# Performance work log

Measured on AMD Instinct MI355X. Metric: run time of the kernel, lower is better.

The kernel has to match this reference:

```python
import jax, jax.numpy as jnp
import numpy as np

N, E, R, D = 100000, 600000, 3, 128  # nodes, edges per relation, relations, hidden


def setup_inputs() -> dict:
    key = jax.random.key(0)
    ks = jax.random.split(key, 12)
    sc = 1.0 / np.sqrt(D)
    return dict(
        x=jax.random.normal(ks[0], (N, D), jnp.float32),
        edge_src=jax.random.randint(ks[1], (R, E), 0, N, jnp.int32),
        edge_dst=jax.random.randint(ks[2], (R, E), 0, N, jnp.int32),
        edge_w=jax.random.uniform(ks[3], (R, E), jnp.float32),
        W=jax.random.normal(ks[4], (R, D, D), jnp.float32) * sc,
        attn_l=jax.random.normal(ks[5], (R, D), jnp.float32) * sc,
        attn_r=jax.random.normal(ks[6], (R, D), jnp.float32) * sc,
        gat_b=jnp.zeros((R, D), jnp.float32),
        bi_w=jax.random.normal(ks[7], (D, D), jnp.float32) * sc,
        bi_b=jnp.zeros((D,), jnp.float32),
        si_w=jax.random.normal(ks[8], (D, D), jnp.float32) * sc,
        si_b=jnp.zeros((D,), jnp.float32),
        res_w=jax.random.normal(ks[9], (), jnp.float32),
        ln_g=jnp.ones((D,), jnp.float32),
        ln_b=jnp.zeros((D,), jnp.float32),
    )


def _leaky(x, slope):
    return jnp.where(x >= 0, x, slope * x)


def _gat(x, W, al, ar, b, src, dst, ew):
    # DGL GATConv, 1 head, edge-weighted: h = xW; e = LReLU(a_l.h_src + a_r.h_dst);
    # alpha = edge_softmax(e per dst) * edge_weight; out[d] = sum alpha * h_src + bias.
    h = x @ W                                   # (N, D)
    el = (h * al).sum(-1)                       # (N,)
    er = (h * ar).sum(-1)                       # (N,)
    e = _leaky(el[src] + er[dst], 0.2)          # (E,)
    m = jax.ops.segment_max(e, dst, num_segments=N)
    a = jnp.exp(e - m[dst])
    s = jax.ops.segment_sum(a, dst, num_segments=N)
    alpha = a / s[dst] * ew                     # (E,)
    out = jax.ops.segment_sum(alpha[:, None] * h[src], dst, num_segments=N)
    return out + b                              # zero-indegree nodes -> bias only


def reference(x, edge_src, edge_dst, edge_w, W, attn_l, attn_r, gat_b,
              bi_w, bi_b, si_w, si_b, res_w, ln_g, ln_b):
    # per-relation intra aggregation, stacked along relation axis: (N, R, D)
    feats = jnp.stack(
        [_gat(x, W[r], attn_l[r], attn_r[r], gat_b[r],
              edge_src[r], edge_dst[r], edge_w[r]) for r in range(R)], axis=1)
    # FM-style bi-interaction over the relation axis
    s = feats.sum(axis=1)                       # (N, D)
    deep_fm = 0.5 * (s ** 2 - (feats ** 2).sum(axis=1))
    nfm = _leaky(deep_fm @ bi_w.T + bi_b, 0.01) + _leaky(s @ si_w.T + si_b, 0.01)
    # gated residual + LayerNorm
    out = nfm + x * jax.nn.sigmoid(res_w)
    mu = out.mean(-1, keepdims=True)
    var = ((out - mu) ** 2).mean(-1, keepdims=True)
    return (out - mu) * jax.lax.rsqrt(var + 1e-5) * ln_g + ln_b
```

## Files before the change

### kernel.cpp

```cpp
#include <hip/hip_runtime.h>

#define DD 128
typedef unsigned int u32;
typedef __attribute__((ext_vector_type(8))) short bf16x8;
typedef __attribute__((ext_vector_type(4))) float f32x4;

__device__ __forceinline__ float lrelu(float v, float s) { return v >= 0.f ? v : s * v; }
__device__ __forceinline__ ushort f2bf(float f) {
  union { float f; u32 u; } v; v.f = f;
  u32 u = v.u;
  return (ushort)((u + 0x7FFFu + ((u >> 16) & 1u)) >> 16);
}
__device__ __forceinline__ float bf2f(ushort s) { return __uint_as_float(((u32)s) << 16); }

union frag_cvt { uint4 u; bf16x8 h; };

__global__ __launch_bounds__(256) void k_prep_w(const float* __restrict__ W,
                                                short* __restrict__ WA)
{
  int t = blockIdx.x * 256 + threadIdx.x;
  int lane = t & 63, ks = (t >> 6) & 3, cf = (t >> 8) & 7, r = t >> 11;
  int c = cf * 16 + (lane & 15);
  int kb = ks * 32 + (lane >> 4) * 8;
  const float* Wr = W + (size_t)r * DD * DD;
  ushort o[8];
#pragma unroll
  for (int j = 0; j < 8; j++) o[j] = f2bf(Wr[(size_t)(kb + j) * DD + c]);
  uint4 st;
  st.x = (u32)o[0] | ((u32)o[1] << 16);
  st.y = (u32)o[2] | ((u32)o[3] << 16);
  st.z = (u32)o[4] | ((u32)o[5] << 16);
  st.w = (u32)o[6] | ((u32)o[7] << 16);
  *(uint4*)(WA + (size_t)t * 8) = st;
}

__global__ __launch_bounds__(256) void k_prep_cw(const float* __restrict__ bw,
                                                 const float* __restrict__ sw,
                                                 short* __restrict__ WB)
{
  int t = blockIdx.x * 256 + threadIdx.x;
  int lane = t & 63, ks = (t >> 6) & 3, cf = (t >> 8) & 7, m = t >> 11;
  const float* src = m ? sw : bw;
  int c = cf * 16 + (lane & 15);
  int k = ks * 32 + (lane >> 4) * 8;
  const float* pr = src + (size_t)c * DD + k;
  uint4 st;
  st.x = (u32)f2bf(pr[0]) | ((u32)f2bf(pr[1]) << 16);
  st.y = (u32)f2bf(pr[2]) | ((u32)f2bf(pr[3]) << 16);
  st.z = (u32)f2bf(pr[4]) | ((u32)f2bf(pr[5]) << 16);
  st.w = (u32)f2bf(pr[6]) | ((u32)f2bf(pr[7]) << 16);
  *(uint4*)(WB + (size_t)t * 8) = st;
}

__global__ void k_prep_av(const float* __restrict__ W, const float* __restrict__ al,
                          const float* __restrict__ ar, float* __restrict__ wl,
                          float* __restrict__ wr)
{
  int t = blockIdx.x * 192 + threadIdx.x;
  if (t >= 384) return;
  int r = t >> 7, k = t & 127;
  const float* Wrow = W + (size_t)r * DD * DD + (size_t)k * DD;
  const float* alr = al + r * DD;
  const float* arr = ar + r * DD;
  float pl = 0.f, pr = 0.f;
  for (int c = 0; c < DD; c++) { float w = Wrow[c]; pl = fmaf(w, alr[c], pl); pr = fmaf(w, arr[c], pr); }
  wl[t] = pl; wr[t] = pr;
}

__global__ __launch_bounds__(256) void k_prep_xrow(
    const float* __restrict__ x, const float* __restrict__ wl, const float* __restrict__ wr,
    u32* __restrict__ xrow, float* __restrict__ el, int2* __restrict__ bex, int N)
{
  const int wid = (int)(((long long)blockIdx.x * 256 + threadIdx.x) >> 6);
  const int lane = threadIdx.x & 63;
  if (wid >= N) return;
  float2 xv = *(const float2*)(x + (size_t)wid * DD + lane * 2);
  xrow[(size_t)wid * 64 + lane] = (u32)f2bf(xv.x) | ((u32)f2bf(xv.y) << 16);
  float d[6];
#pragma unroll
  for (int r = 0; r < 3; r++) {
    float2 wlv = *(const float2*)(wl + r * DD + lane * 2);
    float2 wrv = *(const float2*)(wr + r * DD + lane * 2);
    d[r]     = xv.x * wlv.x + xv.y * wlv.y;
    d[r + 3] = xv.x * wrv.x + xv.y * wrv.y;
  }
#pragma unroll
  for (int o = 32; o; o >>= 1) {
#pragma unroll
    for (int k = 0; k < 6; k++) d[k] += __shfl_xor(d[k], o);
  }
  if (lane == 0) {
#pragma unroll
    for (int r = 0; r < 3; r++) {
      el[(size_t)r * N + wid] = d[r];
      bex[(size_t)r * N + wid].y = __float_as_int(d[r + 3]);
    }
  }
}

__global__ void k_hist3(const int* __restrict__ dst, int* __restrict__ cnt,
                        int* __restrict__ rank, int N, int E) {
  int i = blockIdx.x * 256 + threadIdx.x;
  int r = blockIdx.y;
  if (i < E) {
    size_t ei = (size_t)r * E + i;
    rank[ei] = atomicAdd(cnt + (size_t)r * N + dst[ei], 1);
  }
}

__global__ __launch_bounds__(256) void k_scan_bsum(const int* __restrict__ cnt,
                                                   int* __restrict__ bsum, int M)
{
  __shared__ int red[256];
  const int t = threadIdx.x;
  const int g0 = blockIdx.x * 2048 + t * 8;
  int s = 0;
#pragma unroll
  for (int j = 0; j < 8; j++) { int i = g0 + j; if (i < M) s += cnt[i]; }
  red[t] = s;
  __syncthreads();
  for (int o = 128; o; o >>= 1) {
    if (t < o) red[t] += red[t + o];
    __syncthreads();
  }
  if (t == 0) bsum[blockIdx.x] = red[0];
}

__global__ __launch_bounds__(256) void k_scan_btop(const int* __restrict__ bsum,
                                                   int* __restrict__ bpre, int NB)
{
  __shared__ int sums[256];
  const int t = threadIdx.x;
  int v = (t < NB) ? bsum[t] : 0;
  sums[t] = v;
  __syncthreads();
  for (int o = 1; o < 256; o <<= 1) {
    int u = (t >= o) ? sums[t - o] : 0;
    __syncthreads();
    sums[t] += u;
    __syncthreads();
  }
  if (t < NB) bpre[t] = sums[t] - v;
}

__global__ __launch_bounds__(256) void k_scan_base(const int* __restrict__ cnt,
    const int* __restrict__ bpre, int2* __restrict__ bex, int M)
{
  __shared__ int sums[256];
  const int t = threadIdx.x;
  const int g0 = blockIdx.x * 2048 + t * 8;
  int c[8];
  int ts = 0;
#pragma unroll
  for (int j = 0; j < 8; j++) { int i = g0 + j; c[j] = (i < M) ? cnt[i] : 0; ts += c[j]; }
  sums[t] = ts;
  __syncthreads();
  for (int o = 1; o < 256; o <<= 1) {
    int u = (t >= o) ? sums[t - o] : 0;
    __syncthreads();
    sums[t] += u;
    __syncthreads();
  }
  int run = bpre[blockIdx.x] + sums[t] - ts;
#pragma unroll
  for (int j = 0; j < 8; j++) {
    int i = g0 + j;
    if (i <= M) bex[i].x = run;
    run += c[j];
  }
}

__global__ void k_scatter3(const int* __restrict__ src, const int* __restrict__ dst,
    const float* __restrict__ ew, const float* __restrict__ el,
    const int* __restrict__ rank, const int2* __restrict__ bex,
    int2* __restrict__ meta, int N, int E)
{
  int i = blockIdx.x * 256 + threadIdx.x;
  if (i >= E) return;
  int r = blockIdx.y;
  size_t ei = (size_t)r * E + i;
  int d = dst[ei], s = src[ei];
  int2 be = bex[(size_t)r * N + d];
  int pos = be.x + rank[ei];
  float e = lrelu(el[(size_t)r * N + s] + __int_as_float(be.y), 0.2f);
  meta[pos] = make_int2(s, (int)((u32)f2bf(e) | ((u32)f2bf(ew[ei]) << 16)));
}

__global__ __launch_bounds__(256) void k_node_agg3(
    const int2* __restrict__ bex, const int2* __restrict__ meta,
    const u32* __restrict__ xrow, u32* __restrict__ aggx, int N, int Np)
{
  const int wid = (int)(((long long)blockIdx.x * 256 + threadIdx.x) >> 6);
  const int lane = threadIdx.x & 63;
  if (wid >= N) return;
  const char* xb = (const char*)xrow;
  const int ql = lane & 31, half = lane >> 5;
  const u32 qb = (u32)ql << 3;

  int b0[3], dg[3];
#pragma unroll
  for (int r = 0; r < 3; r++) {
    int v0 = bex[r * N + wid].x;
    int v1 = bex[r * N + wid + 1].x;
    b0[r] = v0; dg[r] = v1 - v0;
  }

  float A0[3] = {0,0,0}, A1[3] = {0,0,0}, A2[3] = {0,0,0}, A3[3] = {0,0,0}, SS[3];

  if (dg[0] <= 64 && dg[1] <= 64 && dg[2] <= 64) {
    int sv[3]; float av[3], cwv[3];
#pragma unroll
    for (int r = 0; r < 3; r++) {
      int s = 0; float a = 0.f, c = 0.f;
      if (lane < dg[r]) {
        int2 mm = meta[b0[r] + lane];
        s = mm.x;
        float e = bf2f((ushort)((u32)mm.y & 0xFFFFu));
        float w = bf2f((ushort)((u32)mm.y >> 16));
        a = __expf(fminf(e, 60.f));
        c = a * w;
      }
      sv[r] = s; av[r] = a; cwv[r] = c;
    }
#pragma unroll
    for (int r = 0; r < 3; r++) {
      float s = av[r];
#pragma unroll
      for (int o = 32; o; o >>= 1) s += __shfl_xor(s, o);
      SS[r] = s;
    }
    float cc[3][4]; u32 so[3][4];
#pragma unroll
    for (int r = 0; r < 3; r++)
#pragma unroll
      for (int q = 0; q < 4; q++) {
        int j = q * 2 + half;
        cc[r][q] = __shfl(cwv[r], j);
        so[r][q] = ((u32)__shfl(sv[r], j) << 8) | qb;
      }
    uint2 uu[3][4];
#pragma unroll
    for (int r = 0; r < 3; r++)
#pragma unroll
      for (int q = 0; q < 4; q++) uu[r][q] = *(const uint2*)(xb + so[r][q]);
#pragma unroll
    for (int r = 0; r < 3; r++)
#pragma unroll
      for (int q = 0; q < 4; q++) {
        A0[r] = fmaf(cc[r][q], __uint_as_float(uu[r][q].x << 16), A0[r]);
        A1[r] = fmaf(cc[r][q], __uint_as_float(uu[r][q].x & 0xFFFF0000u), A1[r]);
        A2[r] = fmaf(cc[r][q], __uint_as_float(uu[r][q].y << 16), A2[r]);
        A3[r] = fmaf(cc[r][q], __uint_as_float(uu[r][q].y & 0xFFFF0000u), A3[r]);
      }
#pragma unroll
    for (int r = 0; r < 3; r++) {
      for (int c8 = 8; c8 < dg[r]; c8 += 8) {
        float c2[4]; u32 o2[4];
#pragma unroll
        for (int q = 0; q < 4; q++) {
          int j = c8 + q * 2 + half;
          c2[q] = __shfl(cwv[r], j);
          o2[q] = ((u32)__shfl(sv[r], j) << 8) | qb;
        }
        uint2 u2[4];
#pragma unroll
        for (int q = 0; q < 4; q++) u2[q] = *(const uint2*)(xb + o2[q]);
#pragma unroll
        for (int q = 0; q < 4; q++) {
          A0[r] = fmaf(c2[q], __uint_as_float(u2[q].x << 16), A0[r]);
          A1[r] = fmaf(c2[q], __uint_as_float(u2[q].x & 0xFFFF0000u), A1[r]);
          A2[r] = fmaf(c2[q], __uint_as_float(u2[q].y << 16), A2[r]);
          A3[r] = fmaf(c2[q], __uint_as_float(u2[q].y & 0xFFFF0000u), A3[r]);
        }
      }
    }
  } else {
#pragma unroll
    for (int r = 0; r < 3; r++) {
      float sp = 0.f;
      for (int c0 = 0; c0 < dg[r]; c0 += 64) {
        int kk = min(64, dg[r] - c0);
        int s = 0; float a = 0.f, c = 0.f;
        if (lane < kk) {
          int2 mm = meta[b0[r] + c0 + lane];
          s = mm.x;
          float e = bf2f((ushort)((u32)mm.y & 0xFFFFu));
          float w = bf2f((ushort)((u32)mm.y >> 16));
          a = __expf(fminf(e, 60.f));
          c = a * w;
        }
        sp += a;
        for (int c8 = 0; c8 < kk; c8 += 8) {
          float c2[4]; u32 o2[4];
#pragma unroll
          for (int q = 0; q < 4; q++) {
            int j = c8 + q * 2 + half;
            c2[q] = __shfl(c, j);
            o2[q] = ((u32)__shfl(s, j) << 8) | qb;
          }
          uint2 u2[4];
#pragma unroll
          for (int q = 0; q < 4; q++) u2[q] = *(const uint2*)(xb + o2[q]);
#pragma unroll
          for (int q = 0; q < 4; q++) {
            A0[r] = fmaf(c2[q], __uint_as_float(u2[q].x << 16), A0[r]);
            A1[r] = fmaf(c2[q], __uint_as_float(u2[q].x & 0xFFFF0000u), A1[r]);
            A2[r] = fmaf(c2[q], __uint_as_float(u2[q].y << 16), A2[r]);
            A3[r] = fmaf(c2[q], __uint_as_float(u2[q].y & 0xFFFF0000u), A3[r]);
          }
        }
      }
#pragma unroll
      for (int o = 32; o; o >>= 1) sp += __shfl_xor(sp, o);
      SS[r] = sp;
    }
  }

#pragma unroll
  for (int r = 0; r < 3; r++) {
    A0[r] += __shfl_xor(A0[r], 32);
    A1[r] += __shfl_xor(A1[r], 32);
    A2[r] += __shfl_xor(A2[r], 32);
    A3[r] += __shfl_xor(A3[r], 32);
  }
  if (half == 0) {
#pragma unroll
    for (int r = 0; r < 3; r++) {
      const float inv = (dg[r] > 0) ? 1.f / SS[r] : 0.f;
      uint2 o;
      o.x = (u32)f2bf(A0[r] * inv) | ((u32)f2bf(A1[r] * inv) << 16);
      o.y = (u32)f2bf(A2[r] * inv) | ((u32)f2bf(A3[r] * inv) << 16);
      *(uint2*)(aggx + ((size_t)r * Np + wid) * 64 + ql * 2) = o;
    }
  }
}

__global__ __launch_bounds__(512) void k_feats(
    const u32* __restrict__ aggx, const short* __restrict__ WA,
    const float* __restrict__ gb, u32* __restrict__ sfrag, u32* __restrict__ dfrag,
    int Np, int ntiles)
{
  extern __shared__ u32 ldsf[];
  u32* lwa = ldsf;
  const int tid = threadIdx.x;
  const int lane = tid & 63;
  const int w = tid >> 6;
  u32* wbuf = ldsf + 24576 + w * 1088;

  for (int i = tid; i < 6144; i += 512)
    *(uint4*)&lwa[i * 4] = *(const uint4*)(WA + (size_t)i * 8);
  __syncthreads();

  const int nl = lane & 15, fh = lane >> 4;

  for (int tile = blockIdx.x; tile < ntiles; tile += gridDim.x) {
    const int tb = tile * 128 + w * 16;
    const int nblk = tile * 8 + w;
    f32x4 sa[8], qa[8];
#pragma unroll
    for (int cf = 0; cf < 8; cf++) { sa[cf] = (f32x4){0,0,0,0}; qa[cf] = (f32x4){0,0,0,0}; }

    for (int r = 0; r < 3; r++) {
#pragma unroll
      for (int rr = 0; rr < 16; rr++)
        wbuf[rr * 68 + lane] = aggx[((size_t)r * Np + tb + rr) * 64 + lane];
      bf16x8 bf[4];
#pragma unroll
      for (int ks = 0; ks < 4; ks++) {
        frag_cvt cv;
        cv.u = *(const uint4*)&wbuf[nl * 68 + ks * 16 + fh * 4];
        bf[ks] = cv.h;
      }
      f32x4 acc[8];
#pragma unroll
      for (int cf = 0; cf < 8; cf++) acc[cf] = (f32x4){0,0,0,0};
#pragma unroll
      for (int ks = 0; ks < 4; ks++) {
#pragma unroll
        for (int cf = 0; cf < 8; cf++) {
          frag_cvt av;
          av.u = *(const uint4*)&lwa[(((r * 8 + cf) * 4 + ks) * 64 + lane) * 4];
          acc[cf] = __builtin_amdgcn_mfma_f32_16x16x32_bf16(av.h, bf[ks], acc[cf], 0, 0, 0);
        }
      }
#pragma unroll
      for (int cf = 0; cf < 8; cf++) {
        float4 g4 = *(const float4*)(gb + r * DD + cf * 16 + fh * 4);
        const float* gp = (const float*)&g4;
#pragma unroll
        for (int j = 0; j < 4; j++) {
          float f = acc[cf][j] + gp[j];
          sa[cf][j] += f;
          qa[cf][j] += f * f;
        }
      }
    }

#pragma unroll
    for (int cf = 0; cf < 8; cf++) {
      int wb = cf * 8 + fh * 2;
      wbuf[nl * 68 + wb]     = (u32)f2bf(sa[cf][0]) | ((u32)f2bf(sa[cf][1]) << 16);
      wbuf[nl * 68 + wb + 1] = (u32)f2bf(sa[cf][2]) | ((u32)f2bf(sa[cf][3]) << 16);
    }
#pragma unroll
    for (int ks = 0; ks < 4; ks++) {
      uint4 v = *(const uint4*)&wbuf[nl * 68 + ks * 16 + fh * 4];
      *(uint4*)&sfrag[(((size_t)nblk * 4 + ks) * 64 + lane) * 4] = v;
    }
#pragma unroll
    for (int cf = 0; cf < 8; cf++) {
      int wb = cf * 8 + fh * 2;
      float d0 = 0.5f * (sa[cf][0] * sa[cf][0] - qa[cf][0]);
      float d1 = 0.5f * (sa[cf][1] * sa[cf][1] - qa[cf][1]);
      float d2 = 0.5f * (sa[cf][2] * sa[cf][2] - qa[cf][2]);
      float d3 = 0.5f * (sa[cf][3] * sa[cf][3] - qa[cf][3]);
      wbuf[nl * 68 + wb]     = (u32)f2bf(d0) | ((u32)f2bf(d1) << 16);
      wbuf[nl * 68 + wb + 1] = (u32)f2bf(d2) | ((u32)f2bf(d3) << 16);
    }
#pragma unroll
    for (int ks = 0; ks < 4; ks++) {
      uint4 v = *(const uint4*)&wbuf[nl * 68 + ks * 16 + fh * 4];
      *(uint4*)&dfrag[(((size_t)nblk * 4 + ks) * 64 + lane) * 4] = v;
    }
  }
}

__global__ __launch_bounds__(512) void k_comb(
    const u32* __restrict__ sfrag, const u32* __restrict__ dfrag,
    const float* __restrict__ x, const short* __restrict__ WB,
    const float* __restrict__ bi_b, const float* __restrict__ si_b,
    const float* __restrict__ res_w, const float* __restrict__ ln_g,
    const float* __restrict__ ln_b, float* __restrict__ out, int N, int ntiles)
{
  extern __shared__ u32 ldsc[];
  u32* lwb = ldsc;
  const int tid = threadIdx.x;
  const int lane = tid & 63;
  const int w = tid >> 6;
  float* obuf = (float*)(ldsc + 16384) + w * 2112;

  for (int i = tid; i < 4096; i += 512)
    *(uint4*)&lwb[i * 4] = *(const uint4*)(WB + (size_t)i * 8);
  __syncthreads();

  const int nl = lane & 15, fh = lane >> 4;
  const float sigw = 1.f / (1.f + __expf(-res_w[0]));
  const float2 g2 = *(const float2*)(ln_g + lane * 2);
  const float2 b2 = *(const float2*)(ln_b + lane * 2);

  for (int tile = blockIdx.x; tile < ntiles; tile += gridDim.x) {
    const int tb = tile * 128 + w * 16;
    const int nblk = tile * 8 + w;
    const int node = tb + nl;

    bf16x8 sf[4], df[4];
#pragma unroll
    for (int ks = 0; ks < 4; ks++) {
      frag_cvt cs, cd;
      cs.u = *(const uint4*)&sfrag[(((size_t)nblk * 4 + ks) * 64 + lane) * 4];
      cd.u = *(const uint4*)&dfrag[(((size_t)nblk * 4 + ks) * 64 + lane) * 4];
      sf[ks] = cs.h; df[ks] = cd.h;
    }
    f32x4 accB[8], accS[8];
#pragma unroll
    for (int cf = 0; cf < 8; cf++) {
      accB[cf] = (f32x4){0,0,0,0};
      accS[cf] = (f32x4){0,0,0,0};
    }
#pragma unroll
    for (int ks = 0; ks < 4; ks++) {
#pragma unroll
      for (int cf = 0; cf < 8; cf++) {
        frag_cvt ab, as;
        ab.u = *(const uint4*)&lwb[(((0 * 8 + cf) * 4 + ks) * 64 + lane) * 4];
        as.u = *(const uint4*)&lwb[(((1 * 8 + cf) * 4 + ks) * 64 + lane) * 4];
        accB[cf] = __builtin_amdgcn_mfma_f32_16x16x32_bf16(ab.h, df[ks], accB[cf], 0, 0, 0);
        accS[cf] = __builtin_amdgcn_mfma_f32_16x16x32_bf16(as.h, sf[ks], accS[cf], 0, 0, 0);
      }
    }

    float sv = 0.f, sq = 0.f;
#pragma unroll
    for (int cf = 0; cf < 8; cf++) {
      int c0 = cf * 16 + fh * 4;
      float4 bb4 = *(const float4*)(bi_b + c0);
      float4 sb4 = *(const float4*)(si_b + c0);
      float4 xv = make_float4(0.f, 0.f, 0.f, 0.f);
      if (node < N) xv = *(const float4*)(x + (size_t)node * DD + c0);
      const float* bbp = (const float*)&bb4;
      const float* sbp = (const float*)&sb4;
      const float* xvp = (const float*)&xv;
      float4 o;
      float* op = (float*)&o;
#pragma unroll
      for (int j = 0; j < 4; j++) {
        float val = lrelu(accB[cf][j] + bbp[j], 0.01f)
                  + lrelu(accS[cf][j] + sbp[j], 0.01f)
                  + xvp[j] * sigw;
        op[j] = val;
        sv += val; sq += val * val;
      }
      *(float4*)&obuf[nl * 132 + c0] = o;
    }
    sv += __shfl_xor(sv, 16); sq += __shfl_xor(sq, 16);
    sv += __shfl_xor(sv, 32); sq += __shfl_xor(sq, 32);
    const float mu = sv * (1.f / DD);
    const float var = sq * (1.f / DD) - mu * mu;
    const float rs = rsqrtf(var + 1e-5f);

#pragma unroll
    for (int rr = 0; rr < 16; rr++) {
      int n2 = tb + rr;
      if (n2 >= N) continue;
      float mur = __shfl(mu, rr);
      float rsr = __shfl(rs, rr);
      float2 v = *(const float2*)&obuf[rr * 132 + lane * 2];
      float2 o;
      o.x = (v.x - mur) * rsr * g2.x + b2.x;
      o.y = (v.y - mur) * rsr * g2.y + b2.y;
      *(float2*)(out + (size_t)n2 * DD + lane * 2) = o;
    }
  }
}

extern "C" void kernel_launch(void* const* d_in, const int* in_sizes, int n_in,
                              void* d_out, int out_size, void* d_ws, size_t ws_size,
                              hipStream_t stream)
{
  const float* x    = (const float*)d_in[0];
  const int*   esrc = (const int*)d_in[1];
  const int*   edst = (const int*)d_in[2];
  const float* ew   = (const float*)d_in[3];
  const float* W    = (const float*)d_in[4];
  const float* al   = (const float*)d_in[5];
  const float* ar   = (const float*)d_in[6];
  const float* gb   = (const float*)d_in[7];
  const float* bi_w = (const float*)d_in[8];
  const float* bi_b = (const float*)d_in[9];
  const float* si_w = (const float*)d_in[10];
  const float* si_b = (const float*)d_in[11];
  const float* res_w= (const float*)d_in[12];
  const float* ln_g = (const float*)d_in[13];
  const float* ln_b = (const float*)d_in[14];

  const int N = in_sizes[0] / DD;
  const int R = 3;
  const int E = in_sizes[1] / R;
  const int Np = ((N + 127) / 128) * 128;
  const int M = R * N;
  const int NB = (M + 2047) / 2048;
  const int ntiles = Np / 128;

  auto al256 = [](size_t v) { return (v + 255) & ~(size_t)255; };
  char* p = (char*)d_ws;
  u32*   xrow  = (u32*)p;
  u32*   sfrag = (u32*)p;
  p += al256((size_t)Np * 64 * 4);
  int*   rank  = (int*)p;
  u32*   aggx  = (u32*)p;
  p += al256((size_t)R * Np * 64 * 4);
  int2*  meta  = (int2*)p; p += al256((size_t)R * E * 8);
  u32*   dfrag = (u32*)p;  p += al256((size_t)Np * 64 * 4);
  float* el    = (float*)p; p += al256((size_t)M * 4);
  int2*  bex   = (int2*)p;  p += al256(((size_t)M + 1) * 8);
  int*   cnt   = (int*)p;   p += al256((size_t)M * 4);
  short* WA    = (short*)p; p += al256((size_t)R * 8 * 4 * 64 * 8 * 2);
  short* WB    = (short*)p; p += al256((size_t)2 * 8 * 4 * 64 * 8 * 2);
  float* wl    = (float*)p; p += al256((size_t)R * DD * 4);
  float* wr    = (float*)p; p += al256((size_t)R * DD * 4);
  int*   bsum  = (int*)p;   p += 1024;
  int*   bpre  = (int*)p;   p += 1024;

  const int egrid = (E + 255) / 256;
  const int DYN_LDS = 133120;

  hipFuncSetAttribute((const void*)k_feats,
                      hipFuncAttributeMaxDynamicSharedMemorySize, DYN_LDS);
  hipFuncSetAttribute((const void*)k_comb,
                      hipFuncAttributeMaxDynamicSharedMemorySize, DYN_LDS);

  k_prep_w<<<24, 256, 0, stream>>>(W, WA);
  k_prep_cw<<<16, 256, 0, stream>>>(bi_w, si_w, WB);
  k_prep_av<<<2, 192, 0, stream>>>(W, al, ar, wl, wr);
  k_prep_xrow<<<(N + 3) / 4, 256, 0, stream>>>(x, wl, wr, xrow, el, bex, N);

  hipMemsetAsync(cnt, 0, (size_t)M * 4, stream);
  k_hist3<<<dim3(egrid, 3), 256, 0, stream>>>(edst, cnt, rank, N, E);
  k_scan_bsum<<<NB, 256, 0, stream>>>(cnt, bsum, M);
  k_scan_btop<<<1, 256, 0, stream>>>(bsum, bpre, NB);
  k_scan_base<<<NB, 256, 0, stream>>>(cnt, bpre, bex, M);
  k_scatter3<<<dim3(egrid, 3), 256, 0, stream>>>(esrc, edst, ew, el, rank, bex,
                                                 meta, N, E);
  k_node_agg3<<<(N + 3) / 4, 256, 0, stream>>>(bex, meta, xrow, aggx, N, Np);
  k_feats<<<256, 512, DYN_LDS, stream>>>(aggx, WA, gb, sfrag, dfrag, Np, ntiles);
  k_comb<<<256, 512, DYN_LDS, stream>>>(sfrag, dfrag, x, WB, bi_b, si_b,
                                        res_w, ln_g, ln_b, (float*)d_out, N, ntiles);
}
```

Baseline: 338.9 us.

## Fuse feats and combine kernels; widen node gather to 16-byte loads

Merges k_feats and k_comb into one k_tail2 kernel, so the sum and FM-interaction fragments stay in registers and are no longer written to and read back from global sfrag/dfrag buffers. The LDS now holds WB plus one relation's WA slice at a time, reloaded per relation inside the tile loop with extra block barriers. Separately, k_node_agg3 now gathers 16-byte chunks per lane, four edges per pass with 8 accumulators per relation, which adds cross-lane shuffle reductions and register pressure. The LayerNorm output is written in two 64-column halves through a smaller per-wave buffer.

```diff
diff --git a/kernel.cpp b/kernel.cpp
--- a/kernel.cpp
+++ b/kernel.cpp
@@ -194,8 +194,8 @@
   const int lane = threadIdx.x & 63;
   if (wid >= N) return;
   const char* xb = (const char*)xrow;
-  const int ql = lane & 31, half = lane >> 5;
-  const u32 qb = (u32)ql << 3;
+  const int ql = lane & 15, q = lane >> 4;
+  const u32 qb = (u32)ql << 4;
 
   int b0[3], dg[3];
 #pragma unroll
@@ -205,7 +205,12 @@
     b0[r] = v0; dg[r] = v1 - v0;
   }
 
-  float A0[3] = {0,0,0}, A1[3] = {0,0,0}, A2[3] = {0,0,0}, A3[3] = {0,0,0}, SS[3];
+  float A[3][8];
+#pragma unroll
+  for (int r = 0; r < 3; r++)
+#pragma unroll
+    for (int i = 0; i < 8; i++) A[r][i] = 0.f;
+  float SS[3];
 
   if (dg[0] <= 64 && dg[1] <= 64 && dg[2] <= 64) {
     int sv[3]; float av[3], cwv[3];
@@ -229,48 +234,58 @@
       for (int o = 32; o; o >>= 1) s += __shfl_xor(s, o);
       SS[r] = s;
     }
-    float cc[3][4]; u32 so[3][4];
+    float cc[3][2]; u32 so[3][2];
 #pragma unroll
     for (int r = 0; r < 3; r++)
 #pragma unroll
-      for (int q = 0; q < 4; q++) {
-        int j = q * 2 + half;
-        cc[r][q] = __shfl(cwv[r], j);
-        so[r][q] = ((u32)__shfl(sv[r], j) << 8) | qb;
-      }
-    uint2 uu[3][4];
+      for (int k = 0; k < 2; k++) {
+        int j = q + k * 4;
+        cc[r][k] = __shfl(cwv[r], j);
+        so[r][k] = ((u32)__shfl(sv[r], j) << 8) | qb;
+      }
+    uint4 uu[3][2];
 #pragma unroll
     for (int r = 0; r < 3; r++)
 #pragma unroll
-      for (int q = 0; q < 4; q++) uu[r][q] = *(const uint2*)(xb + so[r][q]);
+      for (int k = 0; k < 2; k++) uu[r][k] = *(const uint4*)(xb + so[r][k]);
 #pragma unroll
     for (int r = 0; r < 3; r++)
 #pragma unroll
-      for (int q = 0; q < 4; q++) {
-        A0[r] = fmaf(cc[r][q], __uint_as_float(uu[r][q].x << 16), A0[r]);
-        A1[r] = fmaf(cc[r][q], __uint_as_float(uu[r][q].x & 0xFFFF0000u), A1[r]);
-        A2[r] = fmaf(cc[r][q], __uint_as_float(uu[r][q].y << 16), A2[r]);
-        A3[r] = fmaf(cc[r][q], __uint_as_float(uu[r][q].y & 0xFFFF0000u), A3[r]);
+      for (int k = 0; k < 2; k++) {
+        float c = cc[r][k];
+        A[r][0] = fmaf(c, __uint_as_float(uu[r][k].x << 16), A[r][0]);
+        A[r][1] = fmaf(c, __uint_as_float(uu[r][k].x & 0xFFFF0000u), A[r][1]);
+        A[r][2] = fmaf(c, __uint_as_float(uu[r][k].y << 16), A[r][2]);
+        A[r][3] = fmaf(c, __uint_as_float(uu[r][k].y & 0xFFFF0000u), A[r][3]);
+        A[r][4] = fmaf(c, __uint_as_float(uu[r][k].z << 16), A[r][4]);
+        A[r][5] = fmaf(c, __uint_as_float(uu[r][k].z & 0xFFFF0000u), A[r][5]);
+        A[r][6] = fmaf(c, __uint_as_float(uu[r][k].w << 16), A[r][6]);
+        A[r][7] = fmaf(c, __uint_as_float(uu[r][k].w & 0xFFFF0000u), A[r][7]);
       }
 #pragma unroll
     for (int r = 0; r < 3; r++) {
       for (int c8 = 8; c8 < dg[r]; c8 += 8) {
-        float c2[4]; u32 o2[4];
-#pragma unroll
-        for (int q = 0; q < 4; q++) {
-          int j = c8 + q * 2 + half;
-          c2[q] = __shfl(cwv[r], j);
-          o2[q] = ((u32)__shfl(sv[r], j) << 8) | qb;
+        float c2[2]; u32 o2[2];
+#pragma unroll
+        for (int k = 0; k < 2; k++) {
+          int j = c8 + q + k * 4;
+          c2[k] = __shfl(cwv[r], j);
+          o2[k] = ((u32)__shfl(sv[r], j) << 8) | qb;
         }
-        uint2 u2[4];
-#pragma unroll
-        for (int q = 0; q < 4; q++) u2[q] = *(const uint2*)(xb + o2[q]);
-#pragma unroll
-        for (int q = 0; q < 4; q++) {
-          A0[r] = fmaf(c2[q], __uint_as_float(u2[q].x << 16), A0[r]);
-          A1[r] = fmaf(c2[q], __uint_as_float(u2[q].x & 0xFFFF0000u), A1[r]);
-          A2[r] = fmaf(c2[q], __uint_as_float(u2[q].y << 16), A2[r]);
-          A3[r] = fmaf(c2[q], __uint_as_float(u2[q].y & 0xFFFF0000u), A3[r]);
+        uint4 u2[2];
+#pragma unroll
+        for (int k = 0; k < 2; k++) u2[k] = *(const uint4*)(xb + o2[k]);
+#pragma unroll
+        for (int k = 0; k < 2; k++) {
+          float c = c2[k];
+          A[r][0] = fmaf(c, __uint_as_float(u2[k].x << 16), A[r][0]);
+          A[r][1] = fmaf(c, __uint_as_float(u2[k].x & 0xFFFF0000u), A[r][1]);
+          A[r][2] = fmaf(c, __uint_as_float(u2[k].y << 16), A[r][2]);
+          A[r][3] = fmaf(c, __uint_as_float(u2[k].y & 0xFFFF0000u), A[r][3]);
+          A[r][4] = fmaf(c, __uint_as_float(u2[k].z << 16), A[r][4]);
+          A[r][5] = fmaf(c, __uint_as_float(u2[k].z & 0xFFFF0000u), A[r][5]);
+          A[r][6] = fmaf(c, __uint_as_float(u2[k].w << 16), A[r][6]);
+          A[r][7] = fmaf(c, __uint_as_float(u2[k].w & 0xFFFF0000u), A[r][7]);
         }
       }
     }
@@ -291,22 +306,27 @@
         }
         sp += a;
         for (int c8 = 0; c8 < kk; c8 += 8) {
-          float c2[4]; u32 o2[4];
-#pragma unroll
-          for (int q = 0; q < 4; q++) {
-            int j = c8 + q * 2 + half;
-            c2[q] = __shfl(c, j);
-            o2[q] = ((u32)__shfl(s, j) << 8) | qb;
+          float c2[2]; u32 o2[2];
+#pragma unroll
+          for (int k = 0; k < 2; k++) {
+            int j = c8 + q + k * 4;
+            c2[k] = __shfl(c, j);
+            o2[k] = ((u32)__shfl(s, j) << 8) | qb;
           }
-          uint2 u2[4];
-#pragma unroll
-          for (int q = 0; q < 4; q++) u2[q] = *(const uint2*)(xb + o2[q]);
-#pragma unroll
-          for (int q = 0; q < 4; q++) {
-            A0[r] = fmaf(c2[q], __uint_as_float(u2[q].x << 16), A0[r]);
-            A1[r] = fmaf(c2[q], __uint_as_float(u2[q].x & 0xFFFF0000u), A1[r]);
-            A2[r] = fmaf(c2[q], __uint_as_float(u2[q].y << 16), A2[r]);
-            A3[r] = fmaf(c2[q], __uint_as_float(u2[q].y & 0xFFFF0000u), A3[r]);
+          uint4 u2[2];
+#pragma unroll
+          for (int k = 0; k < 2; k++) u2[k] = *(const uint4*)(xb + o2[k]);
+#pragma unroll
+          for (int k = 0; k < 2; k++) {
+            float cx = c2[k];
+            A[r][0] = fmaf(cx, __uint_as_float(u2[k].x << 16), A[r][0]);
+            A[r][1] = fmaf(cx, __uint_as_float(u2[k].x & 0xFFFF0000u), A[r][1]);
+            A[r][2] = fmaf(cx, __uint_as_float(u2[k].y << 16), A[r][2]);
+            A[r][3] = fmaf(cx, __uint_as_float(u2[k].y & 0xFFFF0000u), A[r][3]);
+            A[r][4] = fmaf(cx, __uint_as_float(u2[k].z << 16), A[r][4]);
+            A[r][5] = fmaf(cx, __uint_as_float(u2[k].z & 0xFFFF0000u), A[r][5]);
+            A[r][6] = fmaf(cx, __uint_as_float(u2[k].w << 16), A[r][6]);
+            A[r][7] = fmaf(cx, __uint_as_float(u2[k].w & 0xFFFF0000u), A[r][7]);
           }
         }
       }
@@ -317,50 +337,66 @@
   }
 
 #pragma unroll
-  for (int r = 0; r < 3; r++) {
-    A0[r] += __shfl_xor(A0[r], 32);
-    A1[r] += __shfl_xor(A1[r], 32);
-    A2[r] += __shfl_xor(A2[r], 32);
-    A3[r] += __shfl_xor(A3[r], 32);
-  }
-  if (half == 0) {
+  for (int r = 0; r < 3; r++)
+#pragma unroll
+    for (int i = 0; i < 8; i++) {
+      A[r][i] += __shfl_xor(A[r][i], 32);
+      A[r][i] += __shfl_xor(A[r][i], 16);
+    }
+  if (q == 0) {
 #pragma unroll
     for (int r = 0; r < 3; r++) {
       const float inv = (dg[r] > 0) ? 1.f / SS[r] : 0.f;
-      uint2 o;
-      o.x = (u32)f2bf(A0[r] * inv) | ((u32)f2bf(A1[r] * inv) << 16);
-      o.y = (u32)f2bf(A2[r] * inv) | ((u32)f2bf(A3[r] * inv) << 16);
-      *(uint2*)(aggx + ((size_t)r * Np + wid) * 64 + ql * 2) = o;
-    }
-  }
-}
-
-__global__ __launch_bounds__(512) void k_feats(
+      uint4 o;
+      o.x = (u32)f2bf(A[r][0] * inv) | ((u32)f2bf(A[r][1] * inv) << 16);
+      o.y = (u32)f2bf(A[r][2] * inv) | ((u32)f2bf(A[r][3] * inv) << 16);
+      o.z = (u32)f2bf(A[r][4] * inv) | ((u32)f2bf(A[r][5] * inv) << 16);
+      o.w = (u32)f2bf(A[r][6] * inv) | ((u32)f2bf(A[r][7] * inv) << 16);
+      *(uint4*)(aggx + ((size_t)r * Np + wid) * 64 + ql * 4) = o;
+    }
+  }
+}
+
+__global__ __launch_bounds__(512) void k_tail2(
     const u32* __restrict__ aggx, const short* __restrict__ WA,
-    const float* __restrict__ gb, u32* __restrict__ sfrag, u32* __restrict__ dfrag,
-    int Np, int ntiles)
-{
-  extern __shared__ u32 ldsf[];
-  u32* lwa = ldsf;
+    const short* __restrict__ WB, const float* __restrict__ gb,
+    const float* __restrict__ x,
+    const float* __restrict__ bi_b, const float* __restrict__ si_b,
+    const float* __restrict__ res_w, const float* __restrict__ ln_g,
+    const float* __restrict__ ln_b, float* __restrict__ out,
+    int N, int Np, int ntiles)
+{
+  extern __shared__ u32 lds[];
+  u32* lwb = lds;
+  u32* lwa = lds + 16384;
   const int tid = threadIdx.x;
   const int lane = tid & 63;
   const int w = tid >> 6;
-  u32* wbuf = ldsf + 24576 + w * 1088;
-
-  for (int i = tid; i < 6144; i += 512)
-    *(uint4*)&lwa[i * 4] = *(const uint4*)(WA + (size_t)i * 8);
-  __syncthreads();
+  u32* wbuf = lds + 24576 + w * 1088;
+  float* obuf = (float*)wbuf;
+
+  for (int i = tid; i < 4096; i += 512)
+    *(uint4*)&lwb[i * 4] = *(const uint4*)(WB + (size_t)i * 8);
 
   const int nl = lane & 15, fh = lane >> 4;
+  const float sigw = 1.f / (1.f + __expf(-res_w[0]));
+  const float gA = ln_g[lane], bA = ln_b[lane];
+  const float gB = ln_g[64 + lane], bB = ln_b[64 + lane];
 
   for (int tile = blockIdx.x; tile < ntiles; tile += gridDim.x) {
     const int tb = tile * 128 + w * 16;
-    const int nblk = tile * 8 + w;
+    const int node = tb + nl;
+
     f32x4 sa[8], qa[8];
 #pragma unroll
     for (int cf = 0; cf < 8; cf++) { sa[cf] = (f32x4){0,0,0,0}; qa[cf] = (f32x4){0,0,0,0}; }
 
     for (int r = 0; r < 3; r++) {
+      __syncthreads();
+      for (int i = tid; i < 2048; i += 512)
+        *(uint4*)&lwa[i * 4] = *(const uint4*)(WA + ((size_t)r * 2048 + i) * 8);
+      __syncthreads();
+
 #pragma unroll
       for (int rr = 0; rr < 16; rr++)
         wbuf[rr * 68 + lane] = aggx[((size_t)r * Np + tb + rr) * 64 + lane];
@@ -379,7 +415,7 @@
 #pragma unroll
         for (int cf = 0; cf < 8; cf++) {
           frag_cvt av;
-          av.u = *(const uint4*)&lwa[(((r * 8 + cf) * 4 + ks) * 64 + lane) * 4];
+          av.u = *(const uint4*)&lwa[(((cf) * 4 + ks) * 64 + lane) * 4];
           acc[cf] = __builtin_amdgcn_mfma_f32_16x16x32_bf16(av.h, bf[ks], acc[cf], 0, 0, 0);
         }
       }
@@ -396,6 +432,7 @@
       }
     }
 
+    bf16x8 sf[4], df[4];
 #pragma unroll
     for (int cf = 0; cf < 8; cf++) {
       int wb = cf * 8 + fh * 2;
@@ -404,8 +441,9 @@
     }
 #pragma unroll
     for (int ks = 0; ks < 4; ks++) {
-      uint4 v = *(const uint4*)&wbuf[nl * 68 + ks * 16 + fh * 4];
-      *(uint4*)&sfrag[(((size_t)nblk * 4 + ks) * 64 + lane) * 4] = v;
+      frag_cvt cv;
+      cv.u = *(const uint4*)&wbuf[nl * 68 + ks * 16 + fh * 4];
+      sf[ks] = cv.h;
     }
 #pragma unroll
     for (int cf = 0; cf < 8; cf++) {
@@ -419,48 +457,11 @@
     }
 #pragma unroll
     for (int ks = 0; ks < 4; ks++) {
-      uint4 v = *(const uint4*)&wbuf[nl * 68 + ks * 16 + fh * 4];
-      *(uint4*)&dfrag[(((size_t)nblk * 4 + ks) * 64 + lane) * 4] = v;
-    }
-  }
-}
-
-__global__ __launch_bounds__(512) void k_comb(
-    const u32* __restrict__ sfrag, const u32* __restrict__ dfrag,
-    const float* __restrict__ x, const short* __restrict__ WB,
-    const float* __restrict__ bi_b, const float* __restrict__ si_b,
-    const float* __restrict__ res_w, const float* __restrict__ ln_g,
-    const float* __restrict__ ln_b, float* __restrict__ out, int N, int ntiles)
-{
-  extern __shared__ u32 ldsc[];
-  u32* lwb = ldsc;
-  const int tid = threadIdx.x;
-  const int lane = tid & 63;
-  const int w = tid >> 6;
-  float* obuf = (float*)(ldsc + 16384) + w * 2112;
-
-  for (int i = tid; i < 4096; i += 512)
-    *(uint4*)&lwb[i * 4] = *(const uint4*)(WB + (size_t)i * 8);
-  __syncthreads();
-
-  const int nl = lane & 15, fh = lane >> 4;
-  const float sigw = 1.f / (1.f + __expf(-res_w[0]));
-  const float2 g2 = *(const float2*)(ln_g + lane * 2);
-  const float2 b2 = *(const float2*)(ln_b + lane * 2);
-
-  for (int tile = blockIdx.x; tile < ntiles; tile += gridDim.x) {
-    const int tb = tile * 128 + w * 16;
-    const int nblk = tile * 8 + w;
-    const int node = tb + nl;
-
-    bf16x8 sf[4], df[4];
-#pragma unroll
-    for (int ks = 0; ks < 4; ks++) {
-      frag_cvt cs, cd;
-      cs.u = *(const uint4*)&sfrag[(((size_t)nblk * 4 + ks) * 64 + lane) * 4];
-      cd.u = *(const uint4*)&dfrag[(((size_t)nblk * 4 + ks) * 64 + lane) * 4];
-      sf[ks] = cs.h; df[ks] = cd.h;
-    }
+      frag_cvt cv;
+      cv.u = *(const uint4*)&wbuf[nl * 68 + ks * 16 + fh * 4];
+      df[ks] = cv.h;
+    }
+
     f32x4 accB[8], accS[8];
 #pragma unroll
     for (int cf = 0; cf < 8; cf++) {
@@ -479,6 +480,7 @@
       }
     }
 
+    float4 vals[8];
     float sv = 0.f, sq = 0.f;
 #pragma unroll
     for (int cf = 0; cf < 8; cf++) {
@@ -490,17 +492,15 @@
       const float* bbp = (const float*)&bb4;
       const float* sbp = (const float*)&sb4;
       const float* xvp = (const float*)&xv;
-      float4 o;
-      float* op = (float*)&o;
+      float* vp = (float*)&vals[cf];
 #pragma unroll
       for (int j = 0; j < 4; j++) {
         float val = lrelu(accB[cf][j] + bbp[j], 0.01f)
                   + lrelu(accS[cf][j] + sbp[j], 0.01f)
                   + xvp[j] * sigw;
-        op[j] = val;
+        vp[j] = val;
         sv += val; sq += val * val;
       }
-      *(float4*)&obuf[nl * 132 + c0] = o;
     }
     sv += __shfl_xor(sv, 16); sq += __shfl_xor(sq, 16);
     sv += __shfl_xor(sv, 32); sq += __shfl_xor(sq, 32);
@@ -509,16 +509,21 @@
     const float rs = rsqrtf(var + 1e-5f);
 
 #pragma unroll
-    for (int rr = 0; rr < 16; rr++) {
-      int n2 = tb + rr;
-      if (n2 >= N) continue;
-      float mur = __shfl(mu, rr);
-      float rsr = __shfl(rs, rr);
-      float2 v = *(const float2*)&obuf[rr * 132 + lane * 2];
-      float2 o;
-      o.x = (v.x - mur) * rsr * g2.x + b2.x;
-      o.y = (v.y - mur) * rsr * g2.y + b2.y;
-      *(float2*)(out + (size_t)n2 * DD + lane * 2) = o;
+    for (int half = 0; half < 2; half++) {
+      const float g = half ? gB : gA;
+      const float b = half ? bB : bA;
+#pragma unroll
+      for (int cf = 0; cf < 4; cf++)
+        *(float4*)&obuf[nl * 66 + cf * 16 + fh * 4] = vals[half * 4 + cf];
+#pragma unroll
+      for (int rr = 0; rr < 16; rr++) {
+        int n2 = tb + rr;
+        if (n2 >= N) continue;
+        float mur = __shfl(mu, rr);
+        float rsr = __shfl(rs, rr);
+        float v = obuf[rr * 66 + lane];
+        out[(size_t)n2 * DD + half * 64 + lane] = (v - mur) * rsr * g + b;
+      }
     }
   }
 }
@@ -553,14 +558,11 @@
 
   auto al256 = [](size_t v) { return (v + 255) & ~(size_t)255; };
   char* p = (char*)d_ws;
-  u32*   xrow  = (u32*)p;
-  u32*   sfrag = (u32*)p;
-  p += al256((size_t)Np * 64 * 4);
+  u32*   xrow  = (u32*)p;  p += al256((size_t)Np * 64 * 4);
   int*   rank  = (int*)p;
   u32*   aggx  = (u32*)p;
   p += al256((size_t)R * Np * 64 * 4);
-  int2*  meta  = (int2*)p; p += al256((size_t)R * E * 8);
-  u32*   dfrag = (u32*)p;  p += al256((size_t)Np * 64 * 4);
+  int2*  meta  = (int2*)p;  p += al256((size_t)R * E * 8);
   float* el    = (float*)p; p += al256((size_t)M * 4);
   int2*  bex   = (int2*)p;  p += al256(((size_t)M + 1) * 8);
   int*   cnt   = (int*)p;   p += al256((size_t)M * 4);
@@ -574,9 +576,7 @@
   const int egrid = (E + 255) / 256;
   const int DYN_LDS = 133120;
 
-  hipFuncSetAttribute((const void*)k_feats,
-                      hipFuncAttributeMaxDynamicSharedMemorySize, DYN_LDS);
-  hipFuncSetAttribute((const void*)k_comb,
+  hipFuncSetAttribute((const void*)k_tail2,
                       hipFuncAttributeMaxDynamicSharedMemorySize, DYN_LDS);
 
   k_prep_w<<<24, 256, 0, stream>>>(W, WA);
@@ -592,7 +592,7 @@
   k_scatter3<<<dim3(egrid, 3), 256, 0, stream>>>(esrc, edst, ew, el, rank, bex,
                                                  meta, N, E);
   k_node_agg3<<<(N + 3) / 4, 256, 0, stream>>>(bex, meta, xrow, aggx, N, Np);
-  k_feats<<<256, 512, DYN_LDS, stream>>>(aggx, WA, gb, sfrag, dfrag, Np, ntiles);
-  k_comb<<<256, 512, DYN_LDS, stream>>>(sfrag, dfrag, x, WB, bi_b, si_b,
-                                        res_w, ln_g, ln_b, (float*)d_out, N, ntiles);
-}
+  k_tail2<<<256, 512, DYN_LDS, stream>>>(aggx, WA, WB, gb, x, bi_b, si_b,
+                                         res_w, ln_g, ln_b, (float*)d_out,
+                                         N, Np, ntiles);
+}
```

After: 336.4 us. About the same (-0.7%).

## Fuse relation feature GEMM and combine/LayerNorm kernels into one tail kernel

Applied to the files above, without the earlier changes.

Merges k_feats and k_comb into a single k_tail2 kernel. The summed and bi-interaction bf16 fragments now stay in registers and LDS instead of being written to and re-read from global sfrag/dfrag buffers, which removes that global round trip and one kernel launch. To fit both weight sets in LDS, the per-relation W fragments are reloaded into a 32 KB slot for each relation, with two block-wide barriers per relation per tile. The LayerNorm output path is reworked to stage values in halves through the per-wave buffer and write scalar coalesced stores. The extra barriers and repeated weight reloads, along with higher register pressure, could offset part of the saving.

```diff
diff --git a/kernel.cpp b/kernel.cpp
--- a/kernel.cpp
+++ b/kernel.cpp
@@ -335,32 +335,46 @@
   }
 }
 
-__global__ __launch_bounds__(512) void k_feats(
+__global__ __launch_bounds__(512) void k_tail2(
     const u32* __restrict__ aggx, const short* __restrict__ WA,
-    const float* __restrict__ gb, u32* __restrict__ sfrag, u32* __restrict__ dfrag,
-    int Np, int ntiles)
-{
-  extern __shared__ u32 ldsf[];
-  u32* lwa = ldsf;
+    const short* __restrict__ WB, const float* __restrict__ gb,
+    const float* __restrict__ x,
+    const float* __restrict__ bi_b, const float* __restrict__ si_b,
+    const float* __restrict__ res_w, const float* __restrict__ ln_g,
+    const float* __restrict__ ln_b, float* __restrict__ out,
+    int N, int Np, int ntiles)
+{
+  extern __shared__ u32 lds[];
+  u32* lwb = lds;
+  u32* lwa = lds + 16384;
   const int tid = threadIdx.x;
   const int lane = tid & 63;
   const int w = tid >> 6;
-  u32* wbuf = ldsf + 24576 + w * 1088;
-
-  for (int i = tid; i < 6144; i += 512)
-    *(uint4*)&lwa[i * 4] = *(const uint4*)(WA + (size_t)i * 8);
-  __syncthreads();
+  u32* wbuf = lds + 24576 + w * 1088;
+  float* obuf = (float*)wbuf;
+
+  for (int i = tid; i < 4096; i += 512)
+    *(uint4*)&lwb[i * 4] = *(const uint4*)(WB + (size_t)i * 8);
 
   const int nl = lane & 15, fh = lane >> 4;
+  const float sigw = 1.f / (1.f + __expf(-res_w[0]));
+  const float gA = ln_g[lane], bA = ln_b[lane];
+  const float gB = ln_g[64 + lane], bB = ln_b[64 + lane];
 
   for (int tile = blockIdx.x; tile < ntiles; tile += gridDim.x) {
     const int tb = tile * 128 + w * 16;
-    const int nblk = tile * 8 + w;
+    const int node = tb + nl;
+
     f32x4 sa[8], qa[8];
 #pragma unroll
     for (int cf = 0; cf < 8; cf++) { sa[cf] = (f32x4){0,0,0,0}; qa[cf] = (f32x4){0,0,0,0}; }
 
     for (int r = 0; r < 3; r++) {
+      __syncthreads();
+      for (int i = tid; i < 2048; i += 512)
+        *(uint4*)&lwa[i * 4] = *(const uint4*)(WA + ((size_t)r * 2048 + i) * 8);
+      __syncthreads();
+
 #pragma unroll
       for (int rr = 0; rr < 16; rr++)
         wbuf[rr * 68 + lane] = aggx[((size_t)r * Np + tb + rr) * 64 + lane];
@@ -379,7 +393,7 @@
 #pragma unroll
         for (int cf = 0; cf < 8; cf++) {
           frag_cvt av;
-          av.u = *(const uint4*)&lwa[(((r * 8 + cf) * 4 + ks) * 64 + lane) * 4];
+          av.u = *(const uint4*)&lwa[(((cf) * 4 + ks) * 64 + lane) * 4];
           acc[cf] = __builtin_amdgcn_mfma_f32_16x16x32_bf16(av.h, bf[ks], acc[cf], 0, 0, 0);
         }
       }
@@ -396,6 +410,7 @@
       }
     }
 
+    bf16x8 sf[4], df[4];
 #pragma unroll
     for (int cf = 0; cf < 8; cf++) {
       int wb = cf * 8 + fh * 2;
@@ -404,8 +419,9 @@
     }
 #pragma unroll
     for (int ks = 0; ks < 4; ks++) {
-      uint4 v = *(const uint4*)&wbuf[nl * 68 + ks * 16 + fh * 4];
-      *(uint4*)&sfrag[(((size_t)nblk * 4 + ks) * 64 + lane) * 4] = v;
+      frag_cvt cv;
+      cv.u = *(const uint4*)&wbuf[nl * 68 + ks * 16 + fh * 4];
+      sf[ks] = cv.h;
     }
 #pragma unroll
     for (int cf = 0; cf < 8; cf++) {
@@ -419,48 +435,11 @@
     }
 #pragma unroll
     for (int ks = 0; ks < 4; ks++) {
-      uint4 v = *(const uint4*)&wbuf[nl * 68 + ks * 16 + fh * 4];
-      *(uint4*)&dfrag[(((size_t)nblk * 4 + ks) * 64 + lane) * 4] = v;
-    }
-  }
-}
-
-__global__ __launch_bounds__(512) void k_comb(
-    const u32* __restrict__ sfrag, const u32* __restrict__ dfrag,
-    const float* __restrict__ x, const short* __restrict__ WB,
-    const float* __restrict__ bi_b, const float* __restrict__ si_b,
-    const float* __restrict__ res_w, const float* __restrict__ ln_g,
-    const float* __restrict__ ln_b, float* __restrict__ out, int N, int ntiles)
-{
-  extern __shared__ u32 ldsc[];
-  u32* lwb = ldsc;
-  const int tid = threadIdx.x;
-  const int lane = tid & 63;
-  const int w = tid >> 6;
-  float* obuf = (float*)(ldsc + 16384) + w * 2112;
-
-  for (int i = tid; i < 4096; i += 512)
-    *(uint4*)&lwb[i * 4] = *(const uint4*)(WB + (size_t)i * 8);
-  __syncthreads();
-
-  const int nl = lane & 15, fh = lane >> 4;
-  const float sigw = 1.f / (1.f + __expf(-res_w[0]));
-  const float2 g2 = *(const float2*)(ln_g + lane * 2);
-  const float2 b2 = *(const float2*)(ln_b + lane * 2);
-
-  for (int tile = blockIdx.x; tile < ntiles; tile += gridDim.x) {
-    const int tb = tile * 128 + w * 16;
-    const int nblk = tile * 8 + w;
-    const int node = tb + nl;
-
-    bf16x8 sf[4], df[4];
-#pragma unroll
-    for (int ks = 0; ks < 4; ks++) {
-      frag_cvt cs, cd;
-      cs.u = *(const uint4*)&sfrag[(((size_t)nblk * 4 + ks) * 64 + lane) * 4];
-      cd.u = *(const uint4*)&dfrag[(((size_t)nblk * 4 + ks) * 64 + lane) * 4];
-      sf[ks] = cs.h; df[ks] = cd.h;
-    }
+      frag_cvt cv;
+      cv.u = *(const uint4*)&wbuf[nl * 68 + ks * 16 + fh * 4];
+      df[ks] = cv.h;
+    }
+
     f32x4 accB[8], accS[8];
 #pragma unroll
     for (int cf = 0; cf < 8; cf++) {
@@ -479,6 +458,7 @@
       }
     }
 
+    float4 vals[8];
     float sv = 0.f, sq = 0.f;
 #pragma unroll
     for (int cf = 0; cf < 8; cf++) {
@@ -490,17 +470,15 @@
       const float* bbp = (const float*)&bb4;
       const float* sbp = (const float*)&sb4;
       const float* xvp = (const float*)&xv;
-      float4 o;
-      float* op = (float*)&o;
+      float* vp = (float*)&vals[cf];
 #pragma unroll
       for (int j = 0; j < 4; j++) {
         float val = lrelu(accB[cf][j] + bbp[j], 0.01f)
                   + lrelu(accS[cf][j] + sbp[j], 0.01f)
                   + xvp[j] * sigw;
-        op[j] = val;
+        vp[j] = val;
         sv += val; sq += val * val;
       }
-      *(float4*)&obuf[nl * 132 + c0] = o;
     }
     sv += __shfl_xor(sv, 16); sq += __shfl_xor(sq, 16);
     sv += __shfl_xor(sv, 32); sq += __shfl_xor(sq, 32);
@@ -509,16 +487,21 @@
     const float rs = rsqrtf(var + 1e-5f);
 
 #pragma unroll
-    for (int rr = 0; rr < 16; rr++) {
-      int n2 = tb + rr;
-      if (n2 >= N) continue;
-      float mur = __shfl(mu, rr);
-      float rsr = __shfl(rs, rr);
-      float2 v = *(const float2*)&obuf[rr * 132 + lane * 2];
-      float2 o;
-      o.x = (v.x - mur) * rsr * g2.x + b2.x;
-      o.y = (v.y - mur) * rsr * g2.y + b2.y;
-      *(float2*)(out + (size_t)n2 * DD + lane * 2) = o;
+    for (int half = 0; half < 2; half++) {
+      const float g = half ? gB : gA;
+      const float b = half ? bB : bA;
+#pragma unroll
+      for (int cf = 0; cf < 4; cf++)
+        *(float4*)&obuf[nl * 66 + cf * 16 + fh * 4] = vals[half * 4 + cf];
+#pragma unroll
+      for (int rr = 0; rr < 16; rr++) {
+        int n2 = tb + rr;
+        if (n2 >= N) continue;
+        float mur = __shfl(mu, rr);
+        float rsr = __shfl(rs, rr);
+        float v = obuf[rr * 66 + lane];
+        out[(size_t)n2 * DD + half * 64 + lane] = (v - mur) * rsr * g + b;
+      }
     }
   }
 }
@@ -553,14 +536,11 @@
 
   auto al256 = [](size_t v) { return (v + 255) & ~(size_t)255; };
   char* p = (char*)d_ws;
-  u32*   xrow  = (u32*)p;
-  u32*   sfrag = (u32*)p;
-  p += al256((size_t)Np * 64 * 4);
+  u32*   xrow  = (u32*)p;  p += al256((size_t)Np * 64 * 4);
   int*   rank  = (int*)p;
   u32*   aggx  = (u32*)p;
   p += al256((size_t)R * Np * 64 * 4);
-  int2*  meta  = (int2*)p; p += al256((size_t)R * E * 8);
-  u32*   dfrag = (u32*)p;  p += al256((size_t)Np * 64 * 4);
+  int2*  meta  = (int2*)p;  p += al256((size_t)R * E * 8);
   float* el    = (float*)p; p += al256((size_t)M * 4);
   int2*  bex   = (int2*)p;  p += al256(((size_t)M + 1) * 8);
   int*   cnt   = (int*)p;   p += al256((size_t)M * 4);
@@ -574,9 +554,7 @@
   const int egrid = (E + 255) / 256;
   const int DYN_LDS = 133120;
 
-  hipFuncSetAttribute((const void*)k_feats,
-                      hipFuncAttributeMaxDynamicSharedMemorySize, DYN_LDS);
-  hipFuncSetAttribute((const void*)k_comb,
+  hipFuncSetAttribute((const void*)k_tail2,
                       hipFuncAttributeMaxDynamicSharedMemorySize, DYN_LDS);
 
   k_prep_w<<<24, 256, 0, stream>>>(W, WA);
@@ -592,7 +570,7 @@
   k_scatter3<<<dim3(egrid, 3), 256, 0, stream>>>(esrc, edst, ew, el, rank, bex,
                                                  meta, N, E);
   k_node_agg3<<<(N + 3) / 4, 256, 0, stream>>>(bex, meta, xrow, aggx, N, Np);
-  k_feats<<<256, 512, DYN_LDS, stream>>>(aggx, WA, gb, sfrag, dfrag, Np, ntiles);
-  k_comb<<<256, 512, DYN_LDS, stream>>>(sfrag, dfrag, x, WB, bi_b, si_b,
-                                        res_w, ln_g, ln_b, (float*)d_out, N, ntiles);
-}
+  k_tail2<<<256, 512, DYN_LDS, stream>>>(aggx, WA, WB, gb, x, bi_b, si_b,
+                                         res_w, ln_g, ln_b, (float*)d_out,
+                                         N, Np, ntiles);
+}
```

After: 319.2 us, median of 2. 1.06x faster.
